# Kernel tuning notes

Hardware: AMD Instinct MI355X
Metric: run time of the kernel (lower is better)

The kernel has to match this reference:

```python
import jax, jax.numpy as jnp
import numpy as np

N_NODES = 100000
N_EDGES = 1600000
N_GRAPHS = 128
D = 128          # input_dim == hidden_dim
OUT = 64         # output_dim (num classes)
L = 4            # num_layers - 1 GIN message-passing layers
BN_EPS = 1e-5


def setup_inputs() -> dict:
    key = jax.random.key(0)
    ks = jax.random.split(key, 12)
    s = 1.0 / np.sqrt(D)
    x = jax.random.normal(ks[0], (N_NODES, D), jnp.float32)
    edge_src = jax.random.randint(ks[1], (N_GRAPHS * 0 + N_EDGES,), 0, N_NODES, jnp.int32)
    edge_dst = jax.random.randint(ks[2], (N_EDGES,), 0, N_NODES, jnp.int32)
    graph_ids = jnp.sort(jax.random.randint(ks[3], (N_NODES,), 0, N_GRAPHS, jnp.int32))
    return {
        'x': x,
        'edge_src': edge_src,
        'edge_dst': edge_dst,
        'graph_ids': graph_ids,
        'eps': jnp.zeros((L,), jnp.float32),
        'W1': jax.random.normal(ks[4], (L, D, D), jnp.float32) * s,
        'b1': jnp.zeros((L, D), jnp.float32),
        'g1': jnp.ones((L, D), jnp.float32),
        'be1': jnp.zeros((L, D), jnp.float32),
        'W2': jax.random.normal(ks[5], (L, D, D), jnp.float32) * s,
        'b2': jnp.zeros((L, D), jnp.float32),
        'g2': jnp.ones((L, D), jnp.float32),
        'be2': jnp.zeros((L, D), jnp.float32),
        'predW': jax.random.normal(ks[6], (L + 1, D, OUT), jnp.float32) * s,
        'predb': jnp.zeros((L + 1, OUT), jnp.float32),
    }


def _bn(h, g, b):
    # BatchNorm1d in training mode: batch mean / biased variance over nodes
    mu = jnp.mean(h, axis=0)
    var = jnp.var(h, axis=0)
    return g * (h - mu) * jax.lax.rsqrt(var + BN_EPS) + b


def reference(x, edge_src, edge_dst, graph_ids, eps, W1, b1, g1, be1,
              W2, b2, g2, be2, predW, predb):
    n = x.shape[0]
    hidden = [x]
    h = x
    for l in range(L):
        # sparse Adj @ h : gather neighbor feats at edges, scatter-add to dst
        agg = jax.ops.segment_sum(h[edge_src], edge_dst, num_segments=n)
        pooled = agg + (1.0 + eps[l]) * h                      # GIN eps update
        z = jax.nn.relu(_bn(pooled @ W1[l] + b1[l], g1[l], be1[l]))  # MLP hidden
        z = z @ W2[l] + b2[l]                                  # MLP out
        h = jax.nn.relu(_bn(z, g2[l], be2[l]))                 # outer BN + relu
        hidden.append(h)
    # GIN readout: sum graph pooling + per-layer linear prediction (dropout p=0)
    score = jnp.zeros((N_GRAPHS, OUT), jnp.float32)
    for l, hl in enumerate(hidden):
        pooled_g = jax.ops.segment_sum(hl, graph_ids, num_segments=N_GRAPHS)
        score = score + pooled_g @ predW[l] + predb[l]
    return score
```

## Files before the change

### kernel.cpp

```cpp
#include <hip/hip_runtime.h>

#define NN 100000
#define NE 1600000
#define NG 128
#define DIM 128
#define OUTD 64
#define NL 4
#define SLCAP 48
#define NBKT 391
#define BCAP 6144
#define ECH 4096
#define EBLKS ((NE + ECH - 1) / ECH)

typedef __attribute__((ext_vector_type(8))) short bf16x8;
typedef __attribute__((ext_vector_type(4))) float floatx4;
typedef __attribute__((ext_vector_type(2))) float floatx2;

__device__ __forceinline__ float bf_lo(unsigned u) {
    union { unsigned u; float f; } c; c.u = u << 16; return c.f;
}
__device__ __forceinline__ float bf_hi(unsigned u) {
    union { unsigned u; float f; } c; c.u = u & 0xffff0000u; return c.f;
}
__device__ __forceinline__ unsigned f2bf(float x) {
    union { float f; unsigned u; } c; c.f = x;
    return (c.u + 0x7fffu + ((c.u >> 16) & 1u)) >> 16;
}
__device__ __forceinline__ float bfs2f(short s) {
    union { unsigned u; float f; } c; c.u = ((unsigned)(unsigned short)s) << 16; return c.f;
}

__device__ __forceinline__ void bn_coef(const float* __restrict__ stat,
                                        const float* __restrict__ gamma,
                                        const float* __restrict__ beta,
                                        int f, float& a, float& c) {
    float mu = stat[f] * (1.0f / NN);
    float var = fmaf(-mu, mu, stat[DIM + f] * (1.0f / NN));
    a = gamma[f] * rsqrtf(var + 1e-5f);
    c = fmaf(-mu, a, beta[f]);
}

__global__ __launch_bounds__(256)
void bucketize(const int* __restrict__ esrc, const int* __restrict__ edst,
               int* __restrict__ gcnt, unsigned* __restrict__ bkt) {
    __shared__ int lh[NBKT];
    for (int b = threadIdx.x; b < NBKT; b += 256) lh[b] = 0;
    __syncthreads();
    const int e0 = blockIdx.x * ECH;
    const int e1 = min(e0 + ECH, NE);
    for (int e = e0 + threadIdx.x; e < e1; e += 256)
        atomicAdd(&lh[(unsigned)edst[e] >> 8], 1);
    __syncthreads();
    for (int b = threadIdx.x; b < NBKT; b += 256) {
        int c = lh[b];
        lh[b] = (c > 0) ? atomicAdd(&gcnt[b], c) : 0;
    }
    __syncthreads();
    for (int e = e0 + threadIdx.x; e < e1; e += 256) {
        unsigned d = (unsigned)edst[e];
        unsigned b = d >> 8;
        int p = atomicAdd(&lh[b], 1);
        if (p < BCAP)
            bkt[(size_t)b * BCAP + p] = (unsigned)esrc[e] | ((d & 255u) << 24);
    }
}

__global__ __launch_bounds__(256)
void bucket_to_slots(const unsigned* __restrict__ bkt, const int* __restrict__ gcnt,
                     int* __restrict__ cnt, int* __restrict__ slot) {
    __shared__ int lslot[256 * SLCAP];
    __shared__ int lc[256];
    const int b = blockIdx.x, t = threadIdx.x;
    lc[t] = 0;
    __syncthreads();
    int ne = gcnt[b]; if (ne > BCAP) ne = BCAP;
    const unsigned* be = bkt + (size_t)b * BCAP;
    for (int i = t; i < ne; i += 256) {
        unsigned v = be[i];
        int local = v >> 24;
        int pos = atomicAdd(&lc[local], 1);
        if (pos < SLCAP) lslot[local * SLCAP + pos] = (int)(v & 0xFFFFFFu);
    }
    __syncthreads();
    const int node = b * 256 + t;
    if (node < NN) cnt[node] = min(lc[t], SLCAP);
    const size_t base = (size_t)b * (256 * SLCAP);
    for (int i = t; i < 256 * SLCAP; i += 256)
        slot[base + i] = lslot[i];
}

__global__ void to_bf16(const float* __restrict__ x, unsigned* __restrict__ xb) {
    size_t i = ((size_t)blockIdx.x * 256 + threadIdx.x) * 4;
    float4 v = *(const float4*)(x + i);
    uint2 o;
    o.x = f2bf(v.x) | (f2bf(v.y) << 16);
    o.y = f2bf(v.z) | (f2bf(v.w) << 16);
    *(uint2*)(xb + i / 2) = o;
}

__global__ void build_wt(const float* __restrict__ W1, const float* __restrict__ W2,
                         unsigned short* __restrict__ Wt) {
    int b = blockIdx.x;
    const float* W = ((b & 1) ? W2 : W1) + (size_t)(b >> 1) * DIM * DIM;
    unsigned short* O = Wt + (size_t)b * DIM * DIM;
    int i = blockIdx.y * 2048 + threadIdx.x;
    for (int j = 0; j < 8; ++j, i += 256) {
        int k = i >> 7, n = i & 127;
        O[n * DIM + k] = (unsigned short)f2bf(W[i]);
    }
}

__global__ void csr_agg(const unsigned* __restrict__ hq, const int* __restrict__ cnt,
                        const int* __restrict__ slot, const float* __restrict__ eps, int l,
                        unsigned* __restrict__ outq) {
    const int t = threadIdx.x;
    const int node = blockIdx.x * 4 + (t >> 6);
    const int lane = t & 63;
    const int chunk = lane & 15;
    const int grp = lane >> 4;
    const uint4* __restrict__ h4 = (const uint4*)hq;

    const int deg = cnt[node];

    floatx2 acc[4];
    {
        uint4 sv = h4[(size_t)node * 16 + chunk];
        float e1 = (grp == 0) ? (1.0f + eps[l]) : 0.0f;
        const unsigned* p = (const unsigned*)&sv;
#pragma unroll
        for (int q = 0; q < 4; ++q) {
            floatx2 v; v.x = bf_lo(p[q]); v.y = bf_hi(p[q]);
            acc[q] = e1 * v;
        }
    }

    if (deg > 0) {
        const int iters = (deg + 15) >> 4;
        const int base = node * SLCAP;
        const int hi = base + deg - 1;
        const int j0 = base + grp;
        int idx[4];
#pragma unroll
        for (int q = 0; q < 4; ++q) {
            int j = j0 + q * 4;
            int v = slot[min(j, hi)];
            idx[q] = (j <= hi) ? v : NN;
        }

        for (int it = 0; it < iters; ++it) {
            uint4 u[4];
#pragma unroll
            for (int q = 0; q < 4; ++q) u[q] = h4[(size_t)idx[q] * 16 + chunk];

            if (it + 1 < iters) {
                const int jn = j0 + (it + 1) * 16;
#pragma unroll
                for (int q = 0; q < 4; ++q) {
                    int j = jn + q * 4;
                    int v = slot[min(j, hi)];
                    idx[q] = (j <= hi) ? v : NN;
                }
            }

#pragma unroll
            for (int q = 0; q < 4; ++q) {
                const unsigned* p = (const unsigned*)&u[q];
#pragma unroll
                for (int r = 0; r < 4; ++r) {
                    floatx2 v; v.x = bf_lo(p[r]); v.y = bf_hi(p[r]);
                    acc[r] += v;
                }
            }
        }
    }

#pragma unroll
    for (int r = 0; r < 4; ++r) {
        acc[r].x += __shfl_xor(acc[r].x, 16);
        acc[r].y += __shfl_xor(acc[r].y, 16);
        acc[r].x += __shfl_xor(acc[r].x, 32);
        acc[r].y += __shfl_xor(acc[r].y, 32);
    }
    if (grp == 0) {
        uint4 o;
        unsigned* po = (unsigned*)&o;
#pragma unroll
        for (int r = 0; r < 4; ++r)
            po[r] = f2bf(acc[r].x) | (f2bf(acc[r].y) << 16);
        ((uint4*)outq)[(size_t)node * 16 + chunk] = o;
    }
}

template<int TR>
__global__ __launch_bounds__(256, 2)
void gemm_mfma(const unsigned short* __restrict__ X, const unsigned short* __restrict__ Wt,
               const float* __restrict__ bias,
               const float* __restrict__ stat, const float* __restrict__ gamma,
               const float* __restrict__ beta,
               unsigned short* __restrict__ Y, float* __restrict__ ostat) {
    __shared__ unsigned short Ws[DIM * DIM];
    __shared__ float tatc[2 * DIM];
    float* red = (float*)Ws;
    const int t = threadIdx.x;
    const int w = t >> 6, lane = t & 63;
    const int quad = lane >> 4, m = lane & 15;
    const int rowbase = blockIdx.x * 128 + w * 32;

#pragma unroll
    for (int i = 0; i < 8; ++i) {
        int chunk = t + i * 256;
        int r = chunk >> 4, c = chunk & 15;
        ((uint4*)Ws)[(r << 4) | (c ^ (r & 15))] = ((const uint4*)Wt)[chunk];
    }
    if (TR && t < DIM) {
        float a, c;
        bn_coef(stat, gamma, beta, t, a, c);
        tatc[t] = a; tatc[DIM + t] = c;
    }

    bf16x8 a[2][4];
#pragma unroll
    for (int rt = 0; rt < 2; ++rt) {
        int row = rowbase + rt * 16 + m;
        if (row > NN - 1) row = NN - 1;
        const unsigned short* xr = X + (size_t)row * DIM + quad * 8;
#pragma unroll
        for (int ks = 0; ks < 4; ++ks)
            a[rt][ks] = *(const bf16x8*)(xr + ks * 32);
    }
    __syncthreads();
    if (TR) {
#pragma unroll
        for (int rt = 0; rt < 2; ++rt)
#pragma unroll
            for (int ks = 0; ks < 4; ++ks) {
                int kk = ks * 32 + quad * 8;
                bf16x8 v = a[rt][ks];
#pragma unroll
                for (int j = 0; j < 8; ++j) {
                    float fv = bfs2f(v[j]);
                    fv = fmaxf(fmaf(fv, tatc[kk + j], tatc[DIM + kk + j]), 0.f);
                    v[j] = (short)f2bf(fv);
                }
                a[rt][ks] = v;
            }
    }

    floatx4 acc[2][8];
#pragma unroll
    for (int rt = 0; rt < 2; ++rt)
#pragma unroll
        for (int ct = 0; ct < 8; ++ct) acc[rt][ct] = (floatx4)0.f;

#pragma unroll
    for (int ct = 0; ct < 8; ++ct) {
        const int row = ct * 16 + m;
        const bf16x8* wrow = (const bf16x8*)&Ws[row * DIM];
#pragma unroll
        for (int ks = 0; ks < 4; ++ks) {
            bf16x8 b = wrow[(ks * 4 + quad) ^ m];
            acc[0][ct] = __builtin_amdgcn_mfma_f32_16x16x32_bf16(a[0][ks], b, acc[0][ct], 0, 0, 0);
            acc[1][ct] = __builtin_amdgcn_mfma_f32_16x16x32_bf16(a[1][ks], b, acc[1][ct], 0, 0, 0);
        }
    }

    float sv[8], qv[8];
#pragma unroll
    for (int ct = 0; ct < 8; ++ct) {
        int col = ct * 16 + m;
        float bv = bias[col];
        float s = 0.f, q = 0.f;
#pragma unroll
        for (int rt = 0; rt < 2; ++rt) {
#pragma unroll
            for (int r = 0; r < 4; ++r) {
                int row = rowbase + rt * 16 + quad * 4 + r;
                float val = acc[rt][ct][r] + bv;
                if (row < NN) {
                    Y[(size_t)row * DIM + col] = (unsigned short)f2bf(val);
                    s += val;
                    q = fmaf(val, val, q);
                }
            }
        }
        s += __shfl_xor(s, 16); s += __shfl_xor(s, 32);
        q += __shfl_xor(q, 16); q += __shfl_xor(q, 32);
        sv[ct] = s; qv[ct] = q;
    }
    __syncthreads();
#pragma unroll
    for (int ct = 0; ct < 8; ++ct) {
        int col = ct * 16 + m;
        if (quad == 0) { red[w * 256 + col] = sv[ct]; red[w * 256 + 128 + col] = qv[ct]; }
    }
    __syncthreads();
    if (t < 256) {
        float tot = red[t] + red[256 + t] + red[512 + t] + red[768 + t];
        unsafeAtomicAdd(&ostat[t], tot);
    }
}

template<int TR>
__global__ void pool_nodes(const unsigned* __restrict__ hq, const int* __restrict__ gid,
                           const float* __restrict__ stat, const float* __restrict__ gamma,
                           const float* __restrict__ beta, float* __restrict__ pg) {
    const int lane = threadIdx.x;
    int start = blockIdx.x * 32;
    int end = start + 32;
    if (end > NN) end = NN;
    int f = lane * 2;
    float a0 = 0.f, c0 = 0.f, a1 = 0.f, c1 = 0.f;
    if (TR) {
        bn_coef(stat, gamma, beta, f, a0, c0);
        bn_coef(stat, gamma, beta, f + 1, a1, c1);
    }
    int cur = gid[start];
    float acc0 = 0.f, acc1 = 0.f;
    for (int i = start; i < end; ++i) {
        int g = gid[i];
        if (g != cur) {
            unsafeAtomicAdd(&pg[cur * DIM + f], acc0);
            unsafeAtomicAdd(&pg[cur * DIM + f + 1], acc1);
            acc0 = 0.f; acc1 = 0.f;
            cur = g;
        }
        unsigned u = hq[(size_t)i * 64 + lane];
        float x0 = bf_lo(u), x1 = bf_hi(u);
        if (TR) {
            x0 = fmaxf(fmaf(x0, a0, c0), 0.f);
            x1 = fmaxf(fmaf(x1, a1, c1), 0.f);
        }
        acc0 += x0; acc1 += x1;
    }
    unsafeAtomicAdd(&pg[cur * DIM + f], acc0);
    unsafeAtomicAdd(&pg[cur * DIM + f + 1], acc1);
}

template<int WRITE>
__global__ void norm_pool(const unsigned* __restrict__ hq, const int* __restrict__ gid,
                          const float* __restrict__ stat, const float* __restrict__ gamma,
                          const float* __restrict__ beta,
                          unsigned* __restrict__ outq, float* __restrict__ pg) {
    const int lane = threadIdx.x;
    int start = blockIdx.x * 32;
    int end = start + 32;
    if (end > NN) end = NN;
    int f = lane * 2;
    float a0, c0, a1, c1;
    bn_coef(stat, gamma, beta, f, a0, c0);
    bn_coef(stat, gamma, beta, f + 1, a1, c1);
    int cur = gid[start];
    float acc0 = 0.f, acc1 = 0.f;
    for (int i = start; i < end; ++i) {
        int g = gid[i];
        if (g != cur) {
            unsafeAtomicAdd(&pg[cur * DIM + f], acc0);
            unsafeAtomicAdd(&pg[cur * DIM + f + 1], acc1);
            acc0 = 0.f; acc1 = 0.f;
            cur = g;
        }
        unsigned u = hq[(size_t)i * 64 + lane];
        float x0 = fmaxf(fmaf(bf_lo(u), a0, c0), 0.f);
        float x1 = fmaxf(fmaf(bf_hi(u), a1, c1), 0.f);
        if (WRITE)
            outq[(size_t)i * 64 + lane] = f2bf(x0) | (f2bf(x1) << 16);
        acc0 += x0; acc1 += x1;
    }
    unsafeAtomicAdd(&pg[cur * DIM + f], acc0);
    unsafeAtomicAdd(&pg[cur * DIM + f + 1], acc1);
}

__global__ void final_score(const float* __restrict__ pg, const float* __restrict__ predW,
                            const float* __restrict__ predb, float* __restrict__ out) {
    int g = blockIdx.x;
    int o = threadIdx.x;
    float acc = 0.f;
    for (int l = 0; l <= NL; ++l) {
        acc += predb[l * OUTD + o];
        const float* pgr = pg + ((size_t)l * NG + g) * DIM;
        const float* w = predW + (size_t)l * DIM * OUTD;
#pragma unroll 8
        for (int k = 0; k < DIM; ++k)
            acc = fmaf(pgr[k], w[k * OUTD + o], acc);
    }
    out[g * OUTD + o] = acc;
}

extern "C" void kernel_launch(void* const* d_in, const int* in_sizes, int n_in,
                              void* d_out, int out_size, void* d_ws, size_t ws_size,
                              hipStream_t stream) {
    const float* x     = (const float*)d_in[0];
    const int*   esrc  = (const int*)d_in[1];
    const int*   edst  = (const int*)d_in[2];
    const int*   gid   = (const int*)d_in[3];
    const float* eps   = (const float*)d_in[4];
    const float* W1    = (const float*)d_in[5];
    const float* b1    = (const float*)d_in[6];
    const float* g1    = (const float*)d_in[7];
    const float* be1   = (const float*)d_in[8];
    const float* W2    = (const float*)d_in[9];
    const float* b2    = (const float*)d_in[10];
    const float* g2    = (const float*)d_in[11];
    const float* be2   = (const float*)d_in[12];
    const float* predW = (const float*)d_in[13];
    const float* predb = (const float*)d_in[14];
    float* out = (float*)d_out;

    unsigned short* XB = (unsigned short*)d_ws;
    unsigned short* A  = XB + (size_t)(NN + 1) * DIM;
    unsigned short* B  = A + (size_t)NN * DIM;
    unsigned short* WT = B + (size_t)NN * DIM;
    float* PG    = (float*)(WT + 8 * DIM * DIM);
    float* STATS = PG + 5 * NG * DIM;
    int* GCNT = (int*)(STATS + NL * 512);
    int* CNT  = GCNT + 512;
    int* SLOT = CNT + NN;
    unsigned* BKT = (unsigned*)B;

    hipMemsetAsync(PG, 0, (5 * NG * DIM + NL * 512 + 512) * sizeof(float), stream);
    hipMemsetAsync(XB + (size_t)NN * DIM, 0, DIM * sizeof(unsigned short), stream);

    bucketize<<<EBLKS, 256, 0, stream>>>(esrc, edst, GCNT, BKT);
    bucket_to_slots<<<NBKT, 256, 0, stream>>>(BKT, GCNT, CNT, SLOT);
    to_bf16<<<(NN * DIM) / 1024, 256, 0, stream>>>(x, (unsigned*)XB);
    build_wt<<<dim3(8, 8), 256, 0, stream>>>(W1, W2, WT);

    const int poolBlocks = (NN + 31) / 32;
    const int aggBlocks  = (NN + 3) / 4;
    const int gemmBlocks = (NN + 127) / 128;

    for (int l = 0; l < NL; ++l) {
        float* STATL = STATS + l * 512;
        if (l == 0) {
            pool_nodes<0><<<poolBlocks, 64, 0, stream>>>((const unsigned*)XB, gid,
                                                         nullptr, nullptr, nullptr, PG);
        } else {
            const float* prevS = STATS + (l - 1) * 512 + 256;
            norm_pool<1><<<poolBlocks, 64, 0, stream>>>((const unsigned*)A, gid, prevS,
                                                        g2 + (l - 1) * DIM, be2 + (l - 1) * DIM,
                                                        (unsigned*)XB, PG + l * NG * DIM);
        }
        csr_agg<<<aggBlocks, 256, 0, stream>>>((const unsigned*)XB, CNT, SLOT, eps, l,
                                               (unsigned*)B);
        gemm_mfma<0><<<gemmBlocks, 256, 0, stream>>>(B, WT + (size_t)(2 * l) * DIM * DIM,
                                                     b1 + l * DIM, nullptr, nullptr, nullptr,
                                                     B, STATL);
        gemm_mfma<1><<<gemmBlocks, 256, 0, stream>>>(B, WT + (size_t)(2 * l + 1) * DIM * DIM,
                                                     b2 + l * DIM, STATL, g1 + l * DIM,
                                                     be1 + l * DIM, A, STATL + 256);
    }
    norm_pool<0><<<poolBlocks, 64, 0, stream>>>((const unsigned*)A, gid,
                                                STATS + (NL - 1) * 512 + 256,
                                                g2 + (NL - 1) * DIM, be2 + (NL - 1) * DIM,
                                                nullptr, PG + NL * NG * DIM);
    final_score<<<NG, OUTD, 0, stream>>>(PG, predW, predb, out);
}
```

Before: 795.4 us.

## Process two row tiles per GEMM block and widen pooling blocks

The MFMA GEMM now handles 256 rows per block in two sub-tiles. It prefetches the second tile's A fragments while the first tile's epilogue runs, so the LDS weight load and BN-stat reduction are amortized over twice the rows. The pooling kernels handle 128 nodes per block, read graph ids as int4, and batch four row loads before accumulating, which cuts per-block overhead and atomics. Risks are halved GEMM grid parallelism (391 blocks) and higher register pressure. The int4 gid loads also rely on NN being a multiple of 4, which it is.

Result: faster. 745.9 us (-6.2%).

```diff
diff --git a/kernel.cpp b/kernel.cpp
--- a/kernel.cpp
+++ b/kernel.cpp
@@ -11,6 +11,7 @@
 #define BCAP 6144
 #define ECH 4096
 #define EBLKS ((NE + ECH - 1) / ECH)
+#define NPB 128
 
 typedef __attribute__((ext_vector_type(8))) short bf16x8;
 typedef __attribute__((ext_vector_type(4))) float floatx4;
@@ -204,7 +205,7 @@
     const int t = threadIdx.x;
     const int w = t >> 6, lane = t & 63;
     const int quad = lane >> 4, m = lane & 15;
-    const int rowbase = blockIdx.x * 128 + w * 32;
+    const int rowb0 = blockIdx.x * 256 + w * 32;
 
 #pragma unroll
     for (int i = 0; i < 8; ++i) {
@@ -221,7 +222,7 @@
     bf16x8 a[2][4];
 #pragma unroll
     for (int rt = 0; rt < 2; ++rt) {
-        int row = rowbase + rt * 16 + m;
+        int row = rowb0 + rt * 16 + m;
         if (row > NN - 1) row = NN - 1;
         const unsigned short* xr = X + (size_t)row * DIM + quad * 8;
 #pragma unroll
@@ -229,63 +230,86 @@
             a[rt][ks] = *(const bf16x8*)(xr + ks * 32);
     }
     __syncthreads();
-    if (TR) {
+
+    float sv[8], qv[8];
+#pragma unroll
+    for (int ct = 0; ct < 8; ++ct) { sv[ct] = 0.f; qv[ct] = 0.f; }
+
+    for (int sub = 0; sub < 2; ++sub) {
+        const int rowbase = rowb0 + sub * 128;
+        if (TR) {
+#pragma unroll
+            for (int rt = 0; rt < 2; ++rt)
+#pragma unroll
+                for (int ks = 0; ks < 4; ++ks) {
+                    int kk = ks * 32 + quad * 8;
+                    bf16x8 v = a[rt][ks];
+#pragma unroll
+                    for (int j = 0; j < 8; ++j) {
+                        float fv = bfs2f(v[j]);
+                        fv = fmaxf(fmaf(fv, tatc[kk + j], tatc[DIM + kk + j]), 0.f);
+                        v[j] = (short)f2bf(fv);
+                    }
+                    a[rt][ks] = v;
+                }
+        }
+
+        floatx4 acc[2][8];
 #pragma unroll
         for (int rt = 0; rt < 2; ++rt)
 #pragma unroll
+            for (int ct = 0; ct < 8; ++ct) acc[rt][ct] = (floatx4)0.f;
+
+#pragma unroll
+        for (int ct = 0; ct < 8; ++ct) {
+            const int row = ct * 16 + m;
+            const bf16x8* wrow = (const bf16x8*)&Ws[row * DIM];
+#pragma unroll
             for (int ks = 0; ks < 4; ++ks) {
-                int kk = ks * 32 + quad * 8;
-                bf16x8 v = a[rt][ks];
-#pragma unroll
-                for (int j = 0; j < 8; ++j) {
-                    float fv = bfs2f(v[j]);
-                    fv = fmaxf(fmaf(fv, tatc[kk + j], tatc[DIM + kk + j]), 0.f);
-                    v[j] = (short)f2bf(fv);
+                bf16x8 b = wrow[(ks * 4 + quad) ^ m];
+                acc[0][ct] = __builtin_amdgcn_mfma_f32_16x16x32_bf16(a[0][ks], b, acc[0][ct], 0, 0, 0);
+                acc[1][ct] = __builtin_amdgcn_mfma_f32_16x16x32_bf16(a[1][ks], b, acc[1][ct], 0, 0, 0);
+            }
+        }
+
+        if (sub == 0) {
+#pragma unroll
+            for (int rt = 0; rt < 2; ++rt) {
+                int row = rowb0 + 128 + rt * 16 + m;
+                if (row > NN - 1) row = NN - 1;
+                const unsigned short* xr = X + (size_t)row * DIM + quad * 8;
+#pragma unroll
+                for (int ks = 0; ks < 4; ++ks)
+                    a[rt][ks] = *(const bf16x8*)(xr + ks * 32);
+            }
+        }
+
+#pragma unroll
+        for (int ct = 0; ct < 8; ++ct) {
+            int col = ct * 16 + m;
+            float bv = bias[col];
+            float s = 0.f, q = 0.f;
+#pragma unroll
+            for (int rt = 0; rt < 2; ++rt) {
+#pragma unroll
+                for (int r = 0; r < 4; ++r) {
+                    int row = rowbase + rt * 16 + quad * 4 + r;
+                    float val = acc[rt][ct][r] + bv;
+                    if (row < NN) {
+                        Y[(size_t)row * DIM + col] = (unsigned short)f2bf(val);
+                        s += val;
+                        q = fmaf(val, val, q);
+                    }
                 }
-                a[rt][ks] = v;
-            }
-    }
-
-    floatx4 acc[2][8];
-#pragma unroll
-    for (int rt = 0; rt < 2; ++rt)
-#pragma unroll
-        for (int ct = 0; ct < 8; ++ct) acc[rt][ct] = (floatx4)0.f;
+            }
+            sv[ct] += s; qv[ct] += q;
+        }
+    }
 
 #pragma unroll
     for (int ct = 0; ct < 8; ++ct) {
-        const int row = ct * 16 + m;
-        const bf16x8* wrow = (const bf16x8*)&Ws[row * DIM];
-#pragma unroll
-        for (int ks = 0; ks < 4; ++ks) {
-            bf16x8 b = wrow[(ks * 4 + quad) ^ m];
-            acc[0][ct] = __builtin_amdgcn_mfma_f32_16x16x32_bf16(a[0][ks], b, acc[0][ct], 0, 0, 0);
-            acc[1][ct] = __builtin_amdgcn_mfma_f32_16x16x32_bf16(a[1][ks], b, acc[1][ct], 0, 0, 0);
-        }
-    }
-
-    float sv[8], qv[8];
-#pragma unroll
-    for (int ct = 0; ct < 8; ++ct) {
-        int col = ct * 16 + m;
-        float bv = bias[col];
-        float s = 0.f, q = 0.f;
-#pragma unroll
-        for (int rt = 0; rt < 2; ++rt) {
-#pragma unroll
-            for (int r = 0; r < 4; ++r) {
-                int row = rowbase + rt * 16 + quad * 4 + r;
-                float val = acc[rt][ct][r] + bv;
-                if (row < NN) {
-                    Y[(size_t)row * DIM + col] = (unsigned short)f2bf(val);
-                    s += val;
-                    q = fmaf(val, val, q);
-                }
-            }
-        }
-        s += __shfl_xor(s, 16); s += __shfl_xor(s, 32);
-        q += __shfl_xor(q, 16); q += __shfl_xor(q, 32);
-        sv[ct] = s; qv[ct] = q;
+        sv[ct] += __shfl_xor(sv[ct], 16); sv[ct] += __shfl_xor(sv[ct], 32);
+        qv[ct] += __shfl_xor(qv[ct], 16); qv[ct] += __shfl_xor(qv[ct], 32);
     }
     __syncthreads();
 #pragma unroll
@@ -305,8 +329,8 @@
                            const float* __restrict__ stat, const float* __restrict__ gamma,
                            const float* __restrict__ beta, float* __restrict__ pg) {
     const int lane = threadIdx.x;
-    int start = blockIdx.x * 32;
-    int end = start + 32;
+    int start = blockIdx.x * NPB;
+    int end = start + NPB;
     if (end > NN) end = NN;
     int f = lane * 2;
     float a0 = 0.f, c0 = 0.f, a1 = 0.f, c1 = 0.f;
@@ -316,21 +340,27 @@
     }
     int cur = gid[start];
     float acc0 = 0.f, acc1 = 0.f;
-    for (int i = start; i < end; ++i) {
-        int g = gid[i];
-        if (g != cur) {
-            unsafeAtomicAdd(&pg[cur * DIM + f], acc0);
-            unsafeAtomicAdd(&pg[cur * DIM + f + 1], acc1);
-            acc0 = 0.f; acc1 = 0.f;
-            cur = g;
-        }
-        unsigned u = hq[(size_t)i * 64 + lane];
-        float x0 = bf_lo(u), x1 = bf_hi(u);
-        if (TR) {
-            x0 = fmaxf(fmaf(x0, a0, c0), 0.f);
-            x1 = fmaxf(fmaf(x1, a1, c1), 0.f);
-        }
-        acc0 += x0; acc1 += x1;
+    for (int i0 = start; i0 < end; i0 += 4) {
+        int4 g4 = *(const int4*)(gid + i0);
+        unsigned uu[4];
+#pragma unroll
+        for (int k = 0; k < 4; ++k) uu[k] = hq[(size_t)(i0 + k) * 64 + lane];
+        int gg[4] = {g4.x, g4.y, g4.z, g4.w};
+#pragma unroll
+        for (int k = 0; k < 4; ++k) {
+            if (gg[k] != cur) {
+                unsafeAtomicAdd(&pg[cur * DIM + f], acc0);
+                unsafeAtomicAdd(&pg[cur * DIM + f + 1], acc1);
+                acc0 = 0.f; acc1 = 0.f;
+                cur = gg[k];
+            }
+            float x0 = bf_lo(uu[k]), x1 = bf_hi(uu[k]);
+            if (TR) {
+                x0 = fmaxf(fmaf(x0, a0, c0), 0.f);
+                x1 = fmaxf(fmaf(x1, a1, c1), 0.f);
+            }
+            acc0 += x0; acc1 += x1;
+        }
     }
     unsafeAtomicAdd(&pg[cur * DIM + f], acc0);
     unsafeAtomicAdd(&pg[cur * DIM + f + 1], acc1);
@@ -342,8 +372,8 @@
                           const float* __restrict__ beta,
                           unsigned* __restrict__ outq, float* __restrict__ pg) {
     const int lane = threadIdx.x;
-    int start = blockIdx.x * 32;
-    int end = start + 32;
+    int start = blockIdx.x * NPB;
+    int end = start + NPB;
     if (end > NN) end = NN;
     int f = lane * 2;
     float a0, c0, a1, c1;
@@ -351,20 +381,26 @@
     bn_coef(stat, gamma, beta, f + 1, a1, c1);
     int cur = gid[start];
     float acc0 = 0.f, acc1 = 0.f;
-    for (int i = start; i < end; ++i) {
-        int g = gid[i];
-        if (g != cur) {
-            unsafeAtomicAdd(&pg[cur * DIM + f], acc0);
-            unsafeAtomicAdd(&pg[cur * DIM + f + 1], acc1);
-            acc0 = 0.f; acc1 = 0.f;
-            cur = g;
-        }
-        unsigned u = hq[(size_t)i * 64 + lane];
-        float x0 = fmaxf(fmaf(bf_lo(u), a0, c0), 0.f);
-        float x1 = fmaxf(fmaf(bf_hi(u), a1, c1), 0.f);
-        if (WRITE)
-            outq[(size_t)i * 64 + lane] = f2bf(x0) | (f2bf(x1) << 16);
-        acc0 += x0; acc1 += x1;
+    for (int i0 = start; i0 < end; i0 += 4) {
+        int4 g4 = *(const int4*)(gid + i0);
+        unsigned uu[4];
+#pragma unroll
+        for (int k = 0; k < 4; ++k) uu[k] = hq[(size_t)(i0 + k) * 64 + lane];
+        int gg[4] = {g4.x, g4.y, g4.z, g4.w};
+#pragma unroll
+        for (int k = 0; k < 4; ++k) {
+            if (gg[k] != cur) {
+                unsafeAtomicAdd(&pg[cur * DIM + f], acc0);
+                unsafeAtomicAdd(&pg[cur * DIM + f + 1], acc1);
+                acc0 = 0.f; acc1 = 0.f;
+                cur = gg[k];
+            }
+            float x0 = fmaxf(fmaf(bf_lo(uu[k]), a0, c0), 0.f);
+            float x1 = fmaxf(fmaf(bf_hi(uu[k]), a1, c1), 0.f);
+            if (WRITE)
+                outq[(size_t)(i0 + k) * 64 + lane] = f2bf(x0) | (f2bf(x1) << 16);
+            acc0 += x0; acc1 += x1;
+        }
     }
     unsafeAtomicAdd(&pg[cur * DIM + f], acc0);
     unsafeAtomicAdd(&pg[cur * DIM + f + 1], acc1);
@@ -425,9 +461,9 @@
     to_bf16<<<(NN * DIM) / 1024, 256, 0, stream>>>(x, (unsigned*)XB);
     build_wt<<<dim3(8, 8), 256, 0, stream>>>(W1, W2, WT);
 
-    const int poolBlocks = (NN + 31) / 32;
+    const int poolBlocks = (NN + NPB - 1) / NPB;
     const int aggBlocks  = (NN + 3) / 4;
-    const int gemmBlocks = (NN + 127) / 128;
+    const int gemmBlocks = (NN + 255) / 256;
 
     for (int l = 0; l < NL; ++l) {
         float* STATL = STATS + l * 512;
```
